# Kernel optimization log

Hardware: AMD Instinct MI355X
Metric: run time of the kernel (lower is better)

The kernel has to match this reference:

```python
import jax, jax.numpy as jnp
import numpy as np

NEG = -1e30  # log-space 'minus infinity' that stays finite in fp32 arithmetic
BLANK = 0


def _lse3(a, b, c):
    m = jnp.maximum(jnp.maximum(a, b), c)
    return m + jnp.log(jnp.exp(a - m) + jnp.exp(b - m) + jnp.exp(c - m))


def setup_inputs() -> dict:
    key = jax.random.key(0)
    k1, k2, k3, k4 = jax.random.split(key, 4)
    B, T, C, L = 16, 512, 4096, 128
    scores = jax.random.normal(k1, (B, T, C), dtype=jnp.float32)
    labels = jax.random.randint(k2, (B, L), 1, C, dtype=jnp.int64)      # no blanks in targets
    feat_lens = jax.random.randint(k3, (B,), 384, T + 1, dtype=jnp.int64)
    label_lens = jax.random.randint(k4, (B,), 64, L + 1, dtype=jnp.int64)
    return {"scores": scores, "labels": labels, "feat_lens": feat_lens, "label_lens": label_lens}


def reference(scores, labels, feat_lens, label_lens):
    # scores: [B, T, C]. Matches torch: log_softmax then nn.CTCLoss(blank=0,
    # reduction='mean', zero_infinity=True).
    scores = scores.astype(jnp.float32)
    log_probs = jax.nn.log_softmax(scores, axis=-1)                      # [B, T, C]
    B, T, C = scores.shape
    L = labels.shape[1]
    S = 2 * L + 1  # extended label: blank, l1, blank, ..., lL, blank

    ext = jnp.full((B, S), BLANK, dtype=labels.dtype).at[:, 1::2].set(labels)
    # Gather per-(t, extended-symbol) log-probs once: [B, T, S]
    lp = jnp.take_along_axis(log_probs, jnp.broadcast_to(ext[:, None, :], (B, T, S)), axis=2)

    # skip transition s-2 -> s allowed iff ext[s] != blank and ext[s] != ext[s-2]
    skip = jnp.concatenate(
        [jnp.zeros((B, 2), bool), (ext[:, 2:] != ext[:, :-2]) & (ext[:, 2:] != BLANK)], axis=1)

    alpha0 = jnp.full((B, S), NEG, dtype=jnp.float32).at[:, 0].set(lp[:, 0, 0])
    alpha0 = alpha0.at[:, 1].set(jnp.where(label_lens > 0, lp[:, 0, 1], NEG))

    lp_t_first = jnp.swapaxes(lp, 0, 1)  # [T, B, S]

    def step(alpha, xs):
        lp_t, t = xs
        a1 = jnp.pad(alpha, ((0, 0), (1, 0)), constant_values=NEG)[:, :S]
        a2 = jnp.pad(alpha, ((0, 0), (2, 0)), constant_values=NEG)[:, :S]
        a2 = jnp.where(skip, a2, NEG)
        new = lp_t + _lse3(alpha, a1, a2)
        alpha = jnp.where((t < feat_lens)[:, None], new, alpha)  # freeze past feat_len
        return alpha, None

    alpha, _ = jax.lax.scan(step, alpha0, (lp_t_first[1:], jnp.arange(1, T)))

    end = 2 * label_lens  # index of final blank per sample
    a_end = jnp.take_along_axis(alpha, end[:, None], axis=1)[:, 0]
    a_end1 = jnp.where(
        label_lens > 0,
        jnp.take_along_axis(alpha, jnp.maximum(end - 1, 0)[:, None], axis=1)[:, 0], NEG)
    m = jnp.maximum(a_end, a_end1)
    log_lik = m + jnp.log(jnp.exp(a_end - m) + jnp.exp(a_end1 - m))
    loss = -log_lik
    loss = jnp.where(loss > 0.5e30, 0.0, loss)  # zero_infinity=True
    denom = jnp.maximum(label_lens, 1).astype(loss.dtype)
    return jnp.mean(loss / denom)  # torch 'mean': divide by target_lengths, then batch mean
```

## Files before the change

### kernel.cpp

```cpp
#include <hip/hip_runtime.h>

#define T_ 512
#define C_ 4096
#define L_ 128
#define RCPLN2 1.4426950408889634f
#define LN2 0.6931471805599453f
#define NEGL (-1e30f)
#define SCALE_CTR 4.722366482869645e21f
#define SCALE_LOG 72.0f

__device__ __forceinline__ float fexp2(float x) { return __builtin_amdgcn_exp2f(x); }
__device__ __forceinline__ float flog2(float x) { return __builtin_amdgcn_logf(x); }
__device__ __forceinline__ float frcp(float x)  { return __builtin_amdgcn_rcpf(x); }
__device__ __forceinline__ float lg(float x)    { return (x > 0.f) ? flog2(x) : NEGL; }

template <int CTRL>
__device__ __forceinline__ float dppmov(float v) {
  return __int_as_float(__builtin_amdgcn_update_dpp(
      0, __float_as_int(v), CTRL, 0xF, 0xF, true));
}
__device__ __forceinline__ float wshr1(float v) { return dppmov<0x138>(v); }
__device__ __forceinline__ float wshl1(float v) { return dppmov<0x130>(v); }
template <int CTRL>
__device__ __forceinline__ float maxdpp(float v) {
  return fmaxf(v, dppmov<CTRL>(v));
}
__device__ __forceinline__ float wavemax(float v) {
  v = maxdpp<0xB1>(v);
  v = maxdpp<0x4E>(v);
  v = maxdpp<0x141>(v);
  v = maxdpp<0x140>(v);
  v = maxdpp<0x142>(v);
  v = maxdpp<0x143>(v);
  return __int_as_float(__builtin_amdgcn_readlane(__float_as_int(v), 63));
}

__global__ __launch_bounds__(256) void k_lse_gather(
    const float* __restrict__ scores, const int* __restrict__ labels,
    const int* __restrict__ feat_lens,
    float* __restrict__ p_lab, float* __restrict__ p_blank) {
  const int row = blockIdx.x;
  const int b = row >> 9;
  const int t = row & (T_ - 1);
  if (t >= feat_lens[b]) return;

  __shared__ float sRow[C_];
  __shared__ float sSum[4];
  const float4* __restrict__ rp4 = (const float4*)(scores + (size_t)row * C_);
  float4* sRow4 = (float4*)sRow;
  const int tid = threadIdx.x;

  float s0 = 0.f, s1 = 0.f, s2 = 0.f, s3 = 0.f;
#pragma unroll
  for (int k = 0; k < 4; ++k) {
    float4 v = rp4[tid + 256 * k];
    sRow4[tid + 256 * k] = v;
    s0 += fexp2(v.x * RCPLN2);
    s1 += fexp2(v.y * RCPLN2);
    s2 += fexp2(v.z * RCPLN2);
    s3 += fexp2(v.w * RCPLN2);
  }
  float s = (s0 + s1) + (s2 + s3);
#pragma unroll
  for (int off = 32; off; off >>= 1) s += __shfl_down(s, off);
  const int wid = tid >> 6, lane = tid & 63;
  if (lane == 0) sSum[wid] = s;
  __syncthreads();
  const float l2sum = flog2((sSum[0] + sSum[1]) + (sSum[2] + sSum[3]));

  if (tid < L_) {
    const int lab = labels[b * L_ + tid];
    p_lab[(size_t)row * L_ + tid] = fexp2(sRow[lab] * RCPLN2 - l2sum);
  } else if (tid == L_) {
    p_blank[row] = fexp2(sRow[0] * RCPLN2 - l2sum);
  }
}

__global__ __launch_bounds__(128) void k_ctc_dp(
    const float* __restrict__ p_lab, const float* __restrict__ p_blank,
    const int* __restrict__ labels, const int* __restrict__ feat_lens,
    const int* __restrict__ label_lens, float* __restrict__ loss_out) {
  const int b = blockIdx.x;
  const int lane = threadIdx.x & 63;
  const int wid = threadIdx.x >> 6;
  const int flen = feat_lens[b];
  const int llen = label_lens[b];
  const int tm = (flen >> 1) & ~3;

  const int l0 = labels[b * L_ + 2 * lane];
  const int l1 = labels[b * L_ + 2 * lane + 1];
  const int lm1 = __shfl_up(l1, 1);
  const int ln0 = __shfl_down(l0, 1);
  const bool skip1 = (lane > 0) && (l0 != lm1);
  const bool skip3 = (l1 != l0);
  const bool skipd = (lane < 63) && (ln0 != l1);

  const float2* __restrict__ llp = (const float2*)(p_lab + (size_t)b * T_ * L_);
  const float* __restrict__ lpl = p_lab + (size_t)b * T_ * L_;
  const float* __restrict__ lbp = p_blank + b * T_;

  __shared__ float sB[257];
  __shared__ float sSb;

  if (wid == 0) {
    const float2 ll0 = llp[lane];
    float a0 = (lane == 0) ? lbp[0] : 0.f;
    float a1 = (lane == 0) ? ll0.x : 0.f;
    float a2 = 0.f, a3 = 0.f, a4 = 0.f;
    float p = 0.f;
    float Sa = 0.f;

    float2 cc[4], nc[4]; float cb[4], nb[4];
#pragma unroll
    for (int k = 0; k < 4; ++k) {
      cc[k] = llp[(1 + k) * 64 + lane]; cb[k] = lbp[1 + k];
    }
#pragma unroll
    for (int k = 0; k < 4; ++k) {
      const int tt = min(5 + k, flen - 1);
      nc[k] = llp[tt * 64 + lane]; nb[k] = lbp[tt];
    }
    int t = 1;
    while (t <= tm) {
      float2 mc[4]; float mb[4];
#pragma unroll
      for (int k = 0; k < 4; ++k) {
        const int tt = min(t + 8 + k, flen - 1);
        mc[k] = llp[tt * 64 + lane]; mb[k] = lbp[tt];
      }
#pragma unroll
      for (int k = 0; k < 4; ++k) {
        const float n3 = cc[k].y * (a3 + a2 + (skip3 ? a1 : 0.f));
        const float n4 = cb[k] * (a4 + a3);
        const float pn = wshr1(n3);
        const float n0 = cb[k] * (a0 + p);
        const float n1 = cc[k].x * (a1 + a0 + (skip1 ? p : 0.f));
        const float n2 = cb[k] * (a2 + a1);
        a0 = n0; a1 = n1; a2 = n2; a3 = n3;
        a4 = (lane == 63) ? n4 : 0.f;
        p = pn;
        if (k & 1) {
          const float m = wavemax(fmaxf(fmaxf(fmaxf(a0, a1), fmaxf(a2, a3)), a4));
          const float r = frcp(m) * SCALE_CTR;
          Sa += flog2(m) - SCALE_LOG;
          a0 *= r; a1 *= r; a2 *= r; a3 *= r; a4 *= r; p *= r;
        }
      }
#pragma unroll
      for (int k = 0; k < 4; ++k) { cc[k] = nc[k]; cb[k] = nb[k];
                                    nc[k] = mc[k]; nb[k] = mb[k]; }
      t += 4;
    }
    const float2 cce = llp[tm * 64 + lane];
    const float cbe = lbp[tm];
    const float lb2 = flog2(cbe), lc0 = flog2(cce.x), lc1 = flog2(cce.y);
    const float la0 = lg(a0), la1 = lg(a1), la2 = lg(a2), la3 = lg(a3);
    const float la4 = lg(a4);
    __syncthreads();
    float w0 = la0 + sB[4 * lane + 0] - lb2;
    float w1 = la1 + sB[4 * lane + 1] - lc0;
    float w2 = la2 + sB[4 * lane + 2] - lb2;
    float w3 = la3 + sB[4 * lane + 3] - lc1;
    float m = fmaxf(fmaxf(w0, w1), fmaxf(w2, w3));
    float w4 = NEGL;
    if (lane == 63) { w4 = la4 + sB[256] - lb2; m = fmaxf(m, w4); }
#pragma unroll
    for (int off = 1; off < 64; off <<= 1) m = fmaxf(m, __shfl_xor(m, off));
    float sum = fexp2(w0 - m) + fexp2(w1 - m) + fexp2(w2 - m) + fexp2(w3 - m);
    if (lane == 63) sum += fexp2(w4 - m);
#pragma unroll
    for (int off = 1; off < 64; off <<= 1) sum += __shfl_xor(sum, off);
    if (lane == 0) {
      const float l2lik = m + flog2(sum) + Sa + sSb;
      float loss = -LN2 * l2lik;
      if (loss > 0.5e30f || !(loss == loss)) loss = 0.0f;
      loss_out[b] = loss / (float)llen;
    }
  } else {
    const int e = 2 * llen;
    const float ve = lbp[flen - 1];
    const float vo = lpl[(size_t)(flen - 1) * L_ + (llen - 1)];
    float b0 = (4 * lane == e) ? ve : 0.f;
    float b1 = (4 * lane + 1 == e - 1) ? vo : 0.f;
    float b2 = (4 * lane + 2 == e) ? ve : 0.f;
    float b3 = (4 * lane + 3 == e - 1) ? vo : 0.f;
    float b4 = (lane == 63 && e == 256) ? ve : 0.f;
    float q0 = __shfl_down(b0, 1); q0 = (lane == 63) ? b4 : q0;
    float q1 = __shfl_down(b1, 1); q1 = (lane == 63) ? 0.f : q1;
    float Sb = 0.f;

    float2 cc[4], nc[4]; float cb[4], nb[4];
    int t = flen - 2;
#pragma unroll
    for (int k = 0; k < 4; ++k) {
      const int tt = max(t - k, tm);
      cc[k] = llp[tt * 64 + lane]; cb[k] = lbp[tt];
    }
#pragma unroll
    for (int k = 0; k < 4; ++k) {
      const int tt = max(t - 4 - k, tm);
      nc[k] = llp[tt * 64 + lane]; nb[k] = lbp[tt];
    }
    while (t >= tm) {
      float2 mc[4]; float mb[4];
#pragma unroll
      for (int k = 0; k < 4; ++k) {
        const int tt = max(t - 8 - k, tm);
        mc[k] = llp[tt * 64 + lane]; mb[k] = lbp[tt];
      }
#pragma unroll
      for (int k = 0; k < 4; ++k) {
        if (t - k >= tm) {
          const float n0 = cb[k] * (b0 + b1);
          const float n1 = cc[k].x * (b1 + b2 + (skip3 ? b3 : 0.f));
          const float n4 = cb[k] * b4;
          const float q0n = wshl1(n0);
          const float q1n = wshl1(n1);
          const float n3 = cc[k].y * (b3 + q0 + (skipd ? q1 : 0.f));
          const float n2 = cb[k] * (b2 + b3);
          b0 = n0; b1 = n1; b2 = n2; b3 = n3; b4 = n4;
          q0 = (lane == 63) ? n4 : q0n;
          q1 = q1n;
        }
        if (k & 1) {
          const float m = wavemax(fmaxf(fmaxf(fmaxf(b0, b1), fmaxf(b2, b3)), b4));
          const float r = frcp(m) * SCALE_CTR;
          Sb += flog2(m) - SCALE_LOG;
          b0 *= r; b1 *= r; b2 *= r; b3 *= r; b4 *= r; q0 *= r; q1 *= r;
        }
      }
#pragma unroll
      for (int k = 0; k < 4; ++k) { cc[k] = nc[k]; cb[k] = nb[k];
                                    nc[k] = mc[k]; nb[k] = mb[k]; }
      t -= 4;
    }
    sB[4 * lane + 0] = lg(b0);
    sB[4 * lane + 1] = lg(b1);
    sB[4 * lane + 2] = lg(b2);
    sB[4 * lane + 3] = lg(b3);
    if (lane == 63) sB[256] = lg(b4);
    if (lane == 0) sSb = Sb;
    __syncthreads();
  }
}

__global__ __launch_bounds__(64) void k_final(const float* __restrict__ loss_out,
                                              float* __restrict__ out, int B) {
  const int tid = threadIdx.x;
  float v = (tid < B) ? loss_out[tid] : 0.0f;
#pragma unroll
  for (int off = 32; off; off >>= 1) v += __shfl_down(v, off);
  if (tid == 0) out[0] = v / (float)B;
}

extern "C" void kernel_launch(void* const* d_in, const int* in_sizes, int n_in,
                              void* d_out, int out_size, void* d_ws, size_t ws_size,
                              hipStream_t stream) {
  const float* scores = (const float*)d_in[0];
  const int* labels = (const int*)d_in[1];
  const int* feat_lens = (const int*)d_in[2];
  const int* label_lens = (const int*)d_in[3];
  const int B = in_sizes[2];

  float* p_lab = (float*)d_ws;
  float* p_blank = p_lab + (size_t)B * T_ * L_;
  float* loss_out = p_blank + (size_t)B * T_;
  float* out = (float*)d_out;

  k_lse_gather<<<B * T_, 256, 0, stream>>>(scores, labels, feat_lens, p_lab, p_blank);
  k_ctc_dp<<<B, 128, 0, stream>>>(p_lab, p_blank, labels, feat_lens, label_lens, loss_out);
  k_final<<<1, 64, 0, stream>>>(loss_out, out, B);
}
```

Baseline: 219.6 us.

## Fuse softmax-gather, CTC DP and final reduction into one cooperative kernel

Replaces three kernel launches with a single cooperative persistent kernel of 512 blocks. The blocks grid-stride over rows for the log-softmax gather, grid-sync, then run the per-sample alpha/beta DP. The batch mean is done with atomics plus a done-counter instead of a separate final kernel. This removes launch gaps and the separate reduction kernel. The cost is a grid-wide barrier, lower parallelism in the gather phase (512 blocks vs 8192), and a clamp on the rescale max.

Result: slower. 290.9 us (+32.5%).

```diff
diff --git a/kernel.cpp b/kernel.cpp
--- a/kernel.cpp
+++ b/kernel.cpp
@@ -1,8 +1,12 @@
 #include <hip/hip_runtime.h>
+#include <hip/hip_cooperative_groups.h>
+
+namespace cg = cooperative_groups;
 
 #define T_ 512
 #define C_ 4096
 #define L_ 128
+#define GRID_ 512
 #define RCPLN2 1.4426950408889634f
 #define LN2 0.6931471805599453f
 #define NEGL (-1e30f)
@@ -35,54 +39,62 @@
   return __int_as_float(__builtin_amdgcn_readlane(__float_as_int(v), 63));
 }
 
-__global__ __launch_bounds__(256) void k_lse_gather(
+__global__ __launch_bounds__(256, 2) void k_ctc_fused(
     const float* __restrict__ scores, const int* __restrict__ labels,
-    const int* __restrict__ feat_lens,
-    float* __restrict__ p_lab, float* __restrict__ p_blank) {
-  const int row = blockIdx.x;
-  const int b = row >> 9;
-  const int t = row & (T_ - 1);
-  if (t >= feat_lens[b]) return;
-
-  __shared__ float sRow[C_];
-  __shared__ float sSum[4];
-  const float4* __restrict__ rp4 = (const float4*)(scores + (size_t)row * C_);
-  float4* sRow4 = (float4*)sRow;
+    const int* __restrict__ feat_lens, const int* __restrict__ label_lens,
+    int* __restrict__ dpDone, float* __restrict__ lossAcc,
+    float* __restrict__ p_lab, float* __restrict__ p_blank,
+    float* __restrict__ out, int B) {
+  __shared__ __align__(16) float smem[C_ + 8];
   const int tid = threadIdx.x;
-
-  float s0 = 0.f, s1 = 0.f, s2 = 0.f, s3 = 0.f;
-#pragma unroll
-  for (int k = 0; k < 4; ++k) {
-    float4 v = rp4[tid + 256 * k];
-    sRow4[tid + 256 * k] = v;
-    s0 += fexp2(v.x * RCPLN2);
-    s1 += fexp2(v.y * RCPLN2);
-    s2 += fexp2(v.z * RCPLN2);
-    s3 += fexp2(v.w * RCPLN2);
+  const int nrows = B * T_;
+
+  for (int row = blockIdx.x; row < nrows; row += GRID_) {
+    const int b = row >> 9;
+    const int t = row & (T_ - 1);
+    if (t >= feat_lens[b]) continue;
+    float* sRow = smem;
+    float* sSum = smem + C_;
+    const float4* rp4 = (const float4*)(scores + (size_t)row * C_);
+    float4* sRow4 = (float4*)sRow;
+
+    float s0 = 0.f, s1 = 0.f, s2 = 0.f, s3 = 0.f;
+#pragma unroll
+    for (int k = 0; k < 4; ++k) {
+      float4 v = rp4[tid + 256 * k];
+      sRow4[tid + 256 * k] = v;
+      s0 += fexp2(v.x * RCPLN2);
+      s1 += fexp2(v.y * RCPLN2);
+      s2 += fexp2(v.z * RCPLN2);
+      s3 += fexp2(v.w * RCPLN2);
+    }
+    float s = (s0 + s1) + (s2 + s3);
+#pragma unroll
+    for (int off = 32; off; off >>= 1) s += __shfl_down(s, off);
+    const int wid = tid >> 6, lane = tid & 63;
+    if (lane == 0) sSum[wid] = s;
+    __syncthreads();
+    const float l2sum = flog2((sSum[0] + sSum[1]) + (sSum[2] + sSum[3]));
+
+    if (tid < L_) {
+      const int lab = labels[b * L_ + tid];
+      p_lab[(size_t)row * L_ + tid] = fexp2(sRow[lab] * RCPLN2 - l2sum);
+    } else if (tid == L_) {
+      p_blank[row] = fexp2(sRow[0] * RCPLN2 - l2sum);
+    }
+    __syncthreads();
   }
-  float s = (s0 + s1) + (s2 + s3);
-#pragma unroll
-  for (int off = 32; off; off >>= 1) s += __shfl_down(s, off);
-  const int wid = tid >> 6, lane = tid & 63;
-  if (lane == 0) sSum[wid] = s;
-  __syncthreads();
-  const float l2sum = flog2((sSum[0] + sSum[1]) + (sSum[2] + sSum[3]));
-
-  if (tid < L_) {
-    const int lab = labels[b * L_ + tid];
-    p_lab[(size_t)row * L_ + tid] = fexp2(sRow[lab] * RCPLN2 - l2sum);
-  } else if (tid == L_) {
-    p_blank[row] = fexp2(sRow[0] * RCPLN2 - l2sum);
-  }
-}
-
-__global__ __launch_bounds__(128) void k_ctc_dp(
-    const float* __restrict__ p_lab, const float* __restrict__ p_blank,
-    const int* __restrict__ labels, const int* __restrict__ feat_lens,
-    const int* __restrict__ label_lens, float* __restrict__ loss_out) {
+
+  if (blockIdx.x == 0 && tid == 0) { atomicExch(dpDone, 0); atomicExch(lossAcc, 0.0f); }
+
+  cg::this_grid().sync();
+
+  if ((int)blockIdx.x >= B) return;
+  if (tid >= 128) { __syncthreads(); return; }
+
   const int b = blockIdx.x;
-  const int lane = threadIdx.x & 63;
-  const int wid = threadIdx.x >> 6;
+  const int lane = tid & 63;
+  const int wid = tid >> 6;
   const int flen = feat_lens[b];
   const int llen = label_lens[b];
   const int tm = (flen >> 1) & ~3;
@@ -99,8 +111,7 @@
   const float* __restrict__ lpl = p_lab + (size_t)b * T_ * L_;
   const float* __restrict__ lbp = p_blank + b * T_;
 
-  __shared__ float sB[257];
-  __shared__ float sSb;
+  float* sB = smem;
 
   if (wid == 0) {
     const float2 ll0 = llp[lane];
@@ -140,7 +151,8 @@
         a4 = (lane == 63) ? n4 : 0.f;
         p = pn;
         if (k & 1) {
-          const float m = wavemax(fmaxf(fmaxf(fmaxf(a0, a1), fmaxf(a2, a3)), a4));
+          float m = wavemax(fmaxf(fmaxf(fmaxf(a0, a1), fmaxf(a2, a3)), a4));
+          m = fmaxf(m, 1e-35f);
           const float r = frcp(m) * SCALE_CTR;
           Sa += flog2(m) - SCALE_LOG;
           a0 *= r; a1 *= r; a2 *= r; a3 *= r; a4 *= r; p *= r;
@@ -171,10 +183,14 @@
 #pragma unroll
     for (int off = 1; off < 64; off <<= 1) sum += __shfl_xor(sum, off);
     if (lane == 0) {
-      const float l2lik = m + flog2(sum) + Sa + sSb;
+      const float l2lik = m + flog2(sum) + Sa + sB[257];
       float loss = -LN2 * l2lik;
-      if (loss > 0.5e30f || !(loss == loss)) loss = 0.0f;
-      loss_out[b] = loss / (float)llen;
+      if (!(fabsf(loss) < 0.5e30f)) loss = 0.0f;
+      atomicAdd(lossAcc, loss / (float)llen);
+      const int done = __hip_atomic_fetch_add(dpDone, 1, __ATOMIC_ACQ_REL,
+                                              __HIP_MEMORY_SCOPE_AGENT);
+      if (done == B - 1)
+        out[0] = atomicAdd(lossAcc, 0.0f) / (float)B;
     }
   } else {
     const int e = 2 * llen;
@@ -223,7 +239,8 @@
           q1 = q1n;
         }
         if (k & 1) {
-          const float m = wavemax(fmaxf(fmaxf(fmaxf(b0, b1), fmaxf(b2, b3)), b4));
+          float m = wavemax(fmaxf(fmaxf(fmaxf(b0, b1), fmaxf(b2, b3)), b4));
+          m = fmaxf(m, 1e-35f);
           const float r = frcp(m) * SCALE_CTR;
           Sb += flog2(m) - SCALE_LOG;
           b0 *= r; b1 *= r; b2 *= r; b3 *= r; b4 *= r; q0 *= r; q1 *= r;
@@ -239,18 +256,9 @@
     sB[4 * lane + 2] = lg(b2);
     sB[4 * lane + 3] = lg(b3);
     if (lane == 63) sB[256] = lg(b4);
-    if (lane == 0) sSb = Sb;
+    if (lane == 0) sB[257] = Sb;
     __syncthreads();
   }
-}
-
-__global__ __launch_bounds__(64) void k_final(const float* __restrict__ loss_out,
-                                              float* __restrict__ out, int B) {
-  const int tid = threadIdx.x;
-  float v = (tid < B) ? loss_out[tid] : 0.0f;
-#pragma unroll
-  for (int off = 32; off; off >>= 1) v += __shfl_down(v, off);
-  if (tid == 0) out[0] = v / (float)B;
 }
 
 extern "C" void kernel_launch(void* const* d_in, const int* in_sizes, int n_in,
@@ -260,14 +268,17 @@
   const int* labels = (const int*)d_in[1];
   const int* feat_lens = (const int*)d_in[2];
   const int* label_lens = (const int*)d_in[3];
-  const int B = in_sizes[2];
-
-  float* p_lab = (float*)d_ws;
+  int B = in_sizes[2];
+
+  int* dpDone = (int*)d_ws;
+  float* lossAcc = (float*)d_ws + 1;
+  float* p_lab = (float*)d_ws + 64;
   float* p_blank = p_lab + (size_t)B * T_ * L_;
-  float* loss_out = p_blank + (size_t)B * T_;
   float* out = (float*)d_out;
 
-  k_lse_gather<<<B * T_, 256, 0, stream>>>(scores, labels, feat_lens, p_lab, p_blank);
-  k_ctc_dp<<<B, 128, 0, stream>>>(p_lab, p_blank, labels, feat_lens, label_lens, loss_out);
-  k_final<<<1, 64, 0, stream>>>(loss_out, out, B);
-}
+  void* args[] = {(void*)&scores, (void*)&labels, (void*)&feat_lens,
+                  (void*)&label_lens, (void*)&dpDone, (void*)&lossAcc,
+                  (void*)&p_lab, (void*)&p_blank, (void*)&out, (void*)&B};
+  hipLaunchCooperativeKernel((const void*)k_ctc_fused, dim3(GRID_), dim3(256),
+                             args, 0, stream);
+}
```

## Fuse final loss reduction into DP kernel and deepen prefetch pipeline

Applied to the files above, without the earlier changes.

Removes the separate final-reduction kernel. Each DP block now atomically adds its loss, and the last block to finish, found with an agent-scope counter, writes the mean. The counters are reset inside the first kernel. The DP loops also prefetch one more group of four timesteps ahead (three stages instead of two) to hide global-load latency on the serial recurrence. A clamp on the rescale max and a tightened infinity check were added, at the cost of more registers and a nondeterministic summation order.

New measurement: 221.7 us. Within noise of the previous version (+1.0%).

```diff
diff --git a/kernel.cpp b/kernel.cpp
--- a/kernel.cpp
+++ b/kernel.cpp
@@ -38,10 +38,15 @@
 __global__ __launch_bounds__(256) void k_lse_gather(
     const float* __restrict__ scores, const int* __restrict__ labels,
     const int* __restrict__ feat_lens,
-    float* __restrict__ p_lab, float* __restrict__ p_blank) {
+    float* __restrict__ p_lab, float* __restrict__ p_blank,
+    int* __restrict__ dpDone, float* __restrict__ lossAcc) {
   const int row = blockIdx.x;
   const int b = row >> 9;
   const int t = row & (T_ - 1);
+  if (row == 0 && threadIdx.x == 0) {
+    atomicExch(dpDone, 0);
+    atomicExch(lossAcc, 0.0f);
+  }
   if (t >= feat_lens[b]) return;
 
   __shared__ float sRow[C_];
@@ -79,7 +84,8 @@
 __global__ __launch_bounds__(128) void k_ctc_dp(
     const float* __restrict__ p_lab, const float* __restrict__ p_blank,
     const int* __restrict__ labels, const int* __restrict__ feat_lens,
-    const int* __restrict__ label_lens, float* __restrict__ loss_out) {
+    const int* __restrict__ label_lens, int* __restrict__ dpDone,
+    float* __restrict__ lossAcc, float* __restrict__ out, int B) {
   const int b = blockIdx.x;
   const int lane = threadIdx.x & 63;
   const int wid = threadIdx.x >> 6;
@@ -110,7 +116,7 @@
     float p = 0.f;
     float Sa = 0.f;
 
-    float2 cc[4], nc[4]; float cb[4], nb[4];
+    float2 cc[4], nc[4], mc[4]; float cb[4], nb[4], mb[4];
 #pragma unroll
     for (int k = 0; k < 4; ++k) {
       cc[k] = llp[(1 + k) * 64 + lane]; cb[k] = lbp[1 + k];
@@ -120,13 +126,18 @@
       const int tt = min(5 + k, flen - 1);
       nc[k] = llp[tt * 64 + lane]; nb[k] = lbp[tt];
     }
+#pragma unroll
+    for (int k = 0; k < 4; ++k) {
+      const int tt = min(9 + k, flen - 1);
+      mc[k] = llp[tt * 64 + lane]; mb[k] = lbp[tt];
+    }
     int t = 1;
     while (t <= tm) {
-      float2 mc[4]; float mb[4];
-#pragma unroll
-      for (int k = 0; k < 4; ++k) {
-        const int tt = min(t + 8 + k, flen - 1);
-        mc[k] = llp[tt * 64 + lane]; mb[k] = lbp[tt];
+      float2 oc[4]; float ob[4];
+#pragma unroll
+      for (int k = 0; k < 4; ++k) {
+        const int tt = min(t + 12 + k, flen - 1);
+        oc[k] = llp[tt * 64 + lane]; ob[k] = lbp[tt];
       }
 #pragma unroll
       for (int k = 0; k < 4; ++k) {
@@ -140,7 +151,8 @@
         a4 = (lane == 63) ? n4 : 0.f;
         p = pn;
         if (k & 1) {
-          const float m = wavemax(fmaxf(fmaxf(fmaxf(a0, a1), fmaxf(a2, a3)), a4));
+          float m = wavemax(fmaxf(fmaxf(fmaxf(a0, a1), fmaxf(a2, a3)), a4));
+          m = fmaxf(m, 1e-35f);
           const float r = frcp(m) * SCALE_CTR;
           Sa += flog2(m) - SCALE_LOG;
           a0 *= r; a1 *= r; a2 *= r; a3 *= r; a4 *= r; p *= r;
@@ -148,7 +160,8 @@
       }
 #pragma unroll
       for (int k = 0; k < 4; ++k) { cc[k] = nc[k]; cb[k] = nb[k];
-                                    nc[k] = mc[k]; nb[k] = mb[k]; }
+                                    nc[k] = mc[k]; nb[k] = mb[k];
+                                    mc[k] = oc[k]; mb[k] = ob[k]; }
       t += 4;
     }
     const float2 cce = llp[tm * 64 + lane];
@@ -173,8 +186,12 @@
     if (lane == 0) {
       const float l2lik = m + flog2(sum) + Sa + sSb;
       float loss = -LN2 * l2lik;
-      if (loss > 0.5e30f || !(loss == loss)) loss = 0.0f;
-      loss_out[b] = loss / (float)llen;
+      if (!(fabsf(loss) < 0.5e30f)) loss = 0.0f;
+      atomicAdd(lossAcc, loss / (float)llen);
+      const int done = __hip_atomic_fetch_add(dpDone, 1, __ATOMIC_ACQ_REL,
+                                              __HIP_MEMORY_SCOPE_AGENT);
+      if (done == B - 1)
+        out[0] = atomicAdd(lossAcc, 0.0f) / (float)B;
     }
   } else {
     const int e = 2 * llen;
@@ -189,7 +206,7 @@
     float q1 = __shfl_down(b1, 1); q1 = (lane == 63) ? 0.f : q1;
     float Sb = 0.f;
 
-    float2 cc[4], nc[4]; float cb[4], nb[4];
+    float2 cc[4], nc[4], mc[4]; float cb[4], nb[4], mb[4];
     int t = flen - 2;
 #pragma unroll
     for (int k = 0; k < 4; ++k) {
@@ -201,12 +218,17 @@
       const int tt = max(t - 4 - k, tm);
       nc[k] = llp[tt * 64 + lane]; nb[k] = lbp[tt];
     }
+#pragma unroll
+    for (int k = 0; k < 4; ++k) {
+      const int tt = max(t - 8 - k, tm);
+      mc[k] = llp[tt * 64 + lane]; mb[k] = lbp[tt];
+    }
     while (t >= tm) {
-      float2 mc[4]; float mb[4];
-#pragma unroll
-      for (int k = 0; k < 4; ++k) {
-        const int tt = max(t - 8 - k, tm);
-        mc[k] = llp[tt * 64 + lane]; mb[k] = lbp[tt];
+      float2 oc[4]; float ob[4];
+#pragma unroll
+      for (int k = 0; k < 4; ++k) {
+        const int tt = max(t - 12 - k, tm);
+        oc[k] = llp[tt * 64 + lane]; ob[k] = lbp[tt];
       }
 #pragma unroll
       for (int k = 0; k < 4; ++k) {
@@ -223,7 +245,8 @@
           q1 = q1n;
         }
         if (k & 1) {
-          const float m = wavemax(fmaxf(fmaxf(fmaxf(b0, b1), fmaxf(b2, b3)), b4));
+          float m = wavemax(fmaxf(fmaxf(fmaxf(b0, b1), fmaxf(b2, b3)), b4));
+          m = fmaxf(m, 1e-35f);
           const float r = frcp(m) * SCALE_CTR;
           Sb += flog2(m) - SCALE_LOG;
           b0 *= r; b1 *= r; b2 *= r; b3 *= r; b4 *= r; q0 *= r; q1 *= r;
@@ -231,7 +254,8 @@
       }
 #pragma unroll
       for (int k = 0; k < 4; ++k) { cc[k] = nc[k]; cb[k] = nb[k];
-                                    nc[k] = mc[k]; nb[k] = mb[k]; }
+                                    nc[k] = mc[k]; nb[k] = mb[k];
+                                    mc[k] = oc[k]; mb[k] = ob[k]; }
       t -= 4;
     }
     sB[4 * lane + 0] = lg(b0);
@@ -242,15 +266,6 @@
     if (lane == 0) sSb = Sb;
     __syncthreads();
   }
-}
-
-__global__ __launch_bounds__(64) void k_final(const float* __restrict__ loss_out,
-                                              float* __restrict__ out, int B) {
-  const int tid = threadIdx.x;
-  float v = (tid < B) ? loss_out[tid] : 0.0f;
-#pragma unroll
-  for (int off = 32; off; off >>= 1) v += __shfl_down(v, off);
-  if (tid == 0) out[0] = v / (float)B;
 }
 
 extern "C" void kernel_launch(void* const* d_in, const int* in_sizes, int n_in,
@@ -262,12 +277,14 @@
   const int* label_lens = (const int*)d_in[3];
   const int B = in_sizes[2];
 
-  float* p_lab = (float*)d_ws;
+  int* dpDone = (int*)d_ws;
+  float* lossAcc = (float*)d_ws + 1;
+  float* p_lab = (float*)d_ws + 64;
   float* p_blank = p_lab + (size_t)B * T_ * L_;
-  float* loss_out = p_blank + (size_t)B * T_;
   float* out = (float*)d_out;
 
-  k_lse_gather<<<B * T_, 256, 0, stream>>>(scores, labels, feat_lens, p_lab, p_blank);
-  k_ctc_dp<<<B, 128, 0, stream>>>(p_lab, p_blank, labels, feat_lens, label_lens, loss_out);
-  k_final<<<1, 64, 0, stream>>>(loss_out, out, B);
-}
+  k_lse_gather<<<B * T_, 256, 0, stream>>>(scores, labels, feat_lens,
+                                           p_lab, p_blank, dpDone, lossAcc);
+  k_ctc_dp<<<B, 128, 0, stream>>>(p_lab, p_blank, labels, feat_lens, label_lens,
+                                  dpDone, lossAcc, out, B);
+}
```
